# Performance work log

Measured on AMD Instinct MI355X. Metric: run time of the kernel, lower is better.

Reference implementation:

```python
import jax, jax.numpy as jnp
import numpy as np

B, N, E, IN = 16, 4096, 65536, 128
FILTERS = [256, 256, 128]


def setup_inputs() -> dict:
    key = jax.random.key(0)
    ks = jax.random.split(key, 12)
    inp = {
        "x": jax.random.normal(ks[0], (B, N, IN), dtype=jnp.float32),
        "edge_index": jax.random.randint(ks[1], (B, 2, E), 0, N, dtype=jnp.int32),
        "edge_weight": jax.random.uniform(ks[2], (B, E), dtype=jnp.float32),
        "mask": jax.random.randint(ks[3], (B, N), 0, 2, dtype=jnp.int32),
    }
    dims = [IN] + FILTERS
    for i in range(3):
        inp[f"W{i+1}"] = jax.random.normal(ks[4 + 2 * i], (dims[i], dims[i + 1]), dtype=jnp.float32) / np.sqrt(dims[i]).astype(np.float32)
        inp[f"b{i+1}"] = 0.01 * jax.random.normal(ks[5 + 2 * i], (dims[i + 1],), dtype=jnp.float32)
    return inp


def _gcn_layer(x, ei, ew, valid, W, b):
    # GCNConv(add_self_loops=False, normalize=False):
    #   h = x @ W; out[v] = sum_{(u,v)} ew * h[u]; out += b (valid rows only)
    h = x @ W  # [N, d_out]
    u, v = ei[0], ei[1]
    evalid = valid[u] & valid[v]            # drop edges touching masked-out nodes
    w = jnp.where(evalid, ew, 0.0)
    agg = jnp.zeros_like(h).at[v].add(w[:, None] * h[u])
    return jnp.where(valid[:, None], agg + b, 0.0)


def reference(x, edge_index, edge_weight, mask, W1, b1, W2, b2, W3, b3):
    valid = mask > 0  # [B, N] bool
    out = x
    for W, b in ((W1, b1), (W2, b2), (W3, b3)):
        out = jax.vmap(_gcn_layer, in_axes=(0, 0, 0, 0, None, None))(
            out, edge_index, edge_weight, valid, W, b)
        out = jax.nn.relu(out)  # dropout p=0.0 -> identity
    return out
```

## Files before the change

kernel.cpp:

```cpp
#include <hip/hip_runtime.h>

static constexpr int BATCH = 16;
static constexpr int NNODE = 4096;
static constexpr int NEDGE = 65536;
static constexpr int ROWS  = BATCH * NNODE;
static constexpr int CAP   = 2432;
static constexpr int PM    = BATCH * CAP;
static constexpr int DCAP  = 64;

typedef _Float16 half8  __attribute__((ext_vector_type(8)));
typedef _Float16 half4v __attribute__((ext_vector_type(4)));
typedef _Float16 half2v __attribute__((ext_vector_type(2)));
typedef float    f32x4  __attribute__((ext_vector_type(4)));
typedef float    f32x2  __attribute__((ext_vector_type(2)));

__global__ __launch_bounds__(256) void build_kernel(
    const int* __restrict__ ei, const float* __restrict__ ew,
    const int* __restrict__ mask,
    const float* __restrict__ W1, const float* __restrict__ W2,
    const float* __restrict__ W3,
    int* __restrict__ cursor, unsigned int* __restrict__ bkt,
    _Float16* __restrict__ Wt1, _Float16* __restrict__ Wt2,
    _Float16* __restrict__ Wt3,
    int* __restrict__ vlist, int* __restrict__ validN)
{
    __shared__ int sums[256];
    const int blk = blockIdx.x;
    const int t   = threadIdx.x;

    if (blk < 4096) {
        const int idx = blk * 256 + t;
        const int b = idx >> 16;
        const int e = idx & (NEDGE - 1);
        const int* eib = ei + (size_t)b * 2 * NEDGE;
        const int u = eib[e];
        const int v = eib[NEDGE + e];
        const int mrow = b * NNODE;
        if (mask[mrow + u] != 0 && mask[mrow + v] != 0) {
            const _Float16 w = (_Float16)ew[(size_t)b * NEDGE + e];
            const unsigned short wb = __builtin_bit_cast(unsigned short, w);
            const int pos = atomicAdd(&cursor[mrow + v], 1);
            if (pos < DCAP)
                bkt[(size_t)(mrow + v) * DCAP + pos] = ((unsigned)wb << 16) | (unsigned)u;
        }
    } else if (blk < 4608) {
        const int i = (blk - 4096) * 256 + t;
        if (i < 32768) {
            int k = i >> 8, n = i & 255;
            Wt1[n * 128 + k] = (_Float16)W1[i];
        } else if (i < 98304) {
            int j = i - 32768;
            int k = j >> 8, n = j & 255;
            Wt2[n * 256 + k] = (_Float16)W2[j];
        } else {
            int j = i - 98304;
            int k = j >> 7, n = j & 127;
            Wt3[n * 256 + k] = (_Float16)W3[j];
        }
    } else {
        const int b = blk - 4608;
        const int* mb = mask + b * NNODE;
        for (int i = t; i < CAP; i += 256) vlist[b * CAP + i] = 0;

        int loc[16]; int s = 0;
        #pragma unroll
        for (int i = 0; i < 16; ++i) { loc[i] = (mb[t * 16 + i] != 0); s += loc[i]; }
        sums[t] = s;
        __syncthreads();
        for (int off = 1; off < 256; off <<= 1) {
            int v = (t >= off) ? sums[t - off] : 0;
            __syncthreads();
            sums[t] += v;
            __syncthreads();
        }
        int run = (t == 0) ? 0 : sums[t - 1];
        #pragma unroll
        for (int i = 0; i < 16; ++i) {
            const int n = t * 16 + i;
            if (loc[i]) {
                if (run < CAP) vlist[b * CAP + run] = n;
                ++run;
            }
        }
        if (t == 255) validN[b] = run;
    }
}

__global__ __launch_bounds__(256, 4) void fused_g1(
    const unsigned int* __restrict__ bkt, const int* __restrict__ cursor,
    const float* __restrict__ X,
    const int* __restrict__ vlist, const int* __restrict__ validN,
    const _Float16* __restrict__ Wt,
    const float* __restrict__ bias,
    _Float16* __restrict__ Ac)
{
    constexpr int K = 128;
    constexpr int NPAN = 4;
    constexpr int PSTR = 1032;
    constexpr int NW = 64, NI = 4, RST = 72;
    constexpr int NCH = CAP / 32;
    constexpr int ASZ = (NPAN * PSTR) > (4 * 16 * RST) ? (NPAN * PSTR) : (4 * 16 * RST);
    __shared__ _Float16 A16[ASZ];
    __shared__ int s_v[32], s_deg[32];
    __shared__ unsigned s_bk[32][16];

    const int tid  = threadIdx.x;
    const int lane = tid & 63;
    const int wave = tid >> 6;
    const int quad = lane >> 4;
    const int l15  = lane & 15;

    const int xcd  = blockIdx.x & 7;
    const int j    = blockIdx.x >> 3;
    const int batch = 2 * xcd + (j >= NCH);
    const int tile  = (j >= NCH) ? j - NCH : j;
    const int vN   = validN[batch];
    if (tile * 32 >= vN) return;
    const int mrow = batch * NNODE;

    if (tid < 32) {
        const int slot = tile * 32 + tid;
        int v = 0, dg = 0;
        if (slot < vN) {
            v = vlist[batch * CAP + slot];
            dg = cursor[mrow + v];
            dg = dg > DCAP ? DCAP : dg;
        }
        s_v[tid] = v; s_deg[tid] = dg;
    }
    __syncthreads();
    if (tid < 128) {
        const int r = tid >> 2, part = tid & 3;
        const uint4 q = *(const uint4*)&bkt[(size_t)(mrow + s_v[r]) * DCAP + part * 4];
        *(uint4*)&s_bk[r][part * 4] = q;
    }
    __syncthreads();

    const float* Xb = X + (size_t)mrow * 128 + lane * 2;
    for (int r8 = 0; r8 < 8; ++r8) {
        const int r = wave * 8 + r8;
        const int dg = s_deg[r];
        float a0 = 0.0f, a1 = 0.0f;
        if (dg > 0) {
            unsigned pk[16];
            #pragma unroll
            for (int t = 0; t < 16; ++t) pk[t] = s_bk[r][t];
            const unsigned u0 = pk[0] & 0xffffu;
            float wj[16]; float2 xv[16];
            #pragma unroll
            for (int t = 0; t < 16; ++t) {
                const bool ok = (t < dg);
                const unsigned u = ok ? (pk[t] & 0xffffu) : u0;
                wj[t] = ok ? (float)__builtin_bit_cast(_Float16, (unsigned short)(pk[t] >> 16)) : 0.0f;
                xv[t] = *(const float2*)(Xb + (size_t)u * 128);
            }
            #pragma unroll
            for (int t = 0; t < 16; ++t) { a0 += wj[t] * xv[t].x; a1 += wj[t] * xv[t].y; }
            if (dg > 16) {
                const unsigned* bk = bkt + (size_t)(mrow + s_v[r]) * DCAP;
                for (int i = 16; i < dg; ++i) {
                    const unsigned p = bk[i];
                    const float w = (float)__builtin_bit_cast(_Float16, (unsigned short)(p >> 16));
                    const float2 x2 = *(const float2*)(Xb + (size_t)(p & 0xffffu) * 128);
                    a0 += w * x2.x; a1 += w * x2.y;
                }
            }
        }
        half2v o = {(_Float16)a0, (_Float16)a1};
        *(half2v*)&A16[(lane >> 4) * PSTR + r * 32 + ((lane * 2) & 31)] = o;
    }
    __syncthreads();

    f32x4 acc[2][NI];
    #pragma unroll
    for (int mi = 0; mi < 2; ++mi)
        #pragma unroll
        for (int ni = 0; ni < NI; ++ni) acc[mi][ni] = (f32x4)0.0f;

    const _Float16* ap = A16 + l15 * 32 + quad * 8;
    const _Float16* wp = Wt + (size_t)(wave * NW + l15) * K + quad * 8;

    #pragma unroll
    for (int pp = 0; pp < NPAN; ++pp) {
        half8 af[2], bf[NI];
        #pragma unroll
        for (int mi = 0; mi < 2; ++mi)
            af[mi] = *(const half8*)(ap + pp * PSTR + mi * 16 * 32);
        #pragma unroll
        for (int ni = 0; ni < NI; ++ni)
            bf[ni] = *(const half8*)(wp + (size_t)ni * 16 * K + pp * 32);
        #pragma unroll
        for (int mi = 0; mi < 2; ++mi)
            #pragma unroll
            for (int ni = 0; ni < NI; ++ni)
                acc[mi][ni] = __builtin_amdgcn_mfma_f32_16x16x32_f16(
                    bf[ni], af[mi], acc[mi][ni], 0, 0, 0);
    }
    __syncthreads();

    _Float16* stg = A16 + wave * 16 * RST;
    const int rr = lane >> 2;
    const int c0 = lane & 3;
    #pragma unroll
    for (int mi = 0; mi < 2; ++mi) {
        #pragma unroll
        for (int ni = 0; ni < NI; ++ni) {
            f32x4 v = acc[mi][ni];
            const f32x4 bv = *(const f32x4*)&bias[wave * NW + ni * 16 + quad * 4];
            half4v o;
            #pragma unroll
            for (int r = 0; r < 4; ++r) o[r] = (_Float16)fmaxf(v[r] + bv[r], 0.0f);
            *(half4v*)&stg[l15 * RST + ni * 16 + quad * 4] = o;
        }
        const int slot = tile * 32 + mi * 16 + rr;
        if (slot < vN) {
            const int vs = s_v[mi * 16 + rr];
            _Float16* hp2 = &Ac[((size_t)mrow + vs) * 256 + wave * NW];
            #pragma unroll
            for (int c = 0; c < NI / 2; ++c) {
                const int ch = (c0 + 4 * c) * 8;
                half8 v = *(const half8*)&stg[rr * RST + ch];
                *(half8*)(hp2 + ch) = v;
            }
        }
    }
}

__global__ __launch_bounds__(256, 4) void fused_g23(
    const unsigned int* __restrict__ bkt, const int* __restrict__ cursor,
    const _Float16* __restrict__ Ac,
    const int* __restrict__ vlist, const int* __restrict__ validN,
    const _Float16* __restrict__ Wt2,
    const _Float16* __restrict__ Wt3,
    const float* __restrict__ b2,
    _Float16* __restrict__ H3)
{
    constexpr int K    = 256;
    constexpr int NPAN = 8;
    constexpr int PSTR = 1032;
    constexpr int NCH  = CAP / 32;
    __shared__ _Float16 A16[NPAN * PSTR];
    __shared__ int s_v[32], s_deg[32];
    __shared__ unsigned s_bk[32][16];

    const int tid  = threadIdx.x;
    const int lane = tid & 63;
    const int wave = tid >> 6;
    const int quad = lane >> 4;
    const int l15  = lane & 15;

    const int xcd  = blockIdx.x & 7;
    const int j    = blockIdx.x >> 3;
    const int batch = 2 * xcd + (j >= NCH);
    const int tile  = (j >= NCH) ? j - NCH : j;
    const int vN   = validN[batch];
    if (tile * 32 >= vN) return;
    const int mrow = batch * NNODE;

    if (tid < 32) {
        const int slot = tile * 32 + tid;
        int v = 0, dg = 0;
        if (slot < vN) {
            v = vlist[batch * CAP + slot];
            dg = cursor[mrow + v];
            dg = dg > DCAP ? DCAP : dg;
        }
        s_v[tid] = v; s_deg[tid] = dg;
    }
    __syncthreads();
    if (tid < 128) {
        const int r = tid >> 2, part = tid & 3;
        const uint4 q = *(const uint4*)&bkt[(size_t)(mrow + s_v[r]) * DCAP + part * 4];
        *(uint4*)&s_bk[r][part * 4] = q;
    }
    __syncthreads();

    const _Float16* Ab = Ac + (size_t)mrow * 256 + lane * 4;
    for (int r8 = 0; r8 < 8; ++r8) {
        const int r = wave * 8 + r8;
        const int dg = s_deg[r];
        float a0 = 0.0f, a1 = 0.0f, a2 = 0.0f, a3 = 0.0f;
        if (dg > 0) {
            unsigned pk[16];
            #pragma unroll
            for (int t = 0; t < 16; ++t) pk[t] = s_bk[r][t];
            const unsigned u0 = pk[0] & 0xffffu;
            float wj[16]; half4v hv[16];
            #pragma unroll
            for (int t = 0; t < 16; ++t) {
                const bool ok = (t < dg);
                const unsigned u = ok ? (pk[t] & 0xffffu) : u0;
                wj[t] = ok ? (float)__builtin_bit_cast(_Float16, (unsigned short)(pk[t] >> 16)) : 0.0f;
                hv[t] = *(const half4v*)(Ab + (size_t)u * 256);
            }
            #pragma unroll
            for (int t = 0; t < 16; ++t) {
                a0 += wj[t] * (float)hv[t][0];
                a1 += wj[t] * (float)hv[t][1];
                a2 += wj[t] * (float)hv[t][2];
                a3 += wj[t] * (float)hv[t][3];
            }
            if (dg > 16) {
                const unsigned* bk = bkt + (size_t)(mrow + s_v[r]) * DCAP;
                for (int i = 16; i < dg; ++i) {
                    const unsigned p = bk[i];
                    const float w = (float)__builtin_bit_cast(_Float16, (unsigned short)(p >> 16));
                    const half4v h = *(const half4v*)(Ab + (size_t)(p & 0xffffu) * 256);
                    a0 += w * (float)h[0]; a1 += w * (float)h[1];
                    a2 += w * (float)h[2]; a3 += w * (float)h[3];
                }
            }
        }
        half4v o = {(_Float16)a0, (_Float16)a1, (_Float16)a2, (_Float16)a3};
        *(half4v*)&A16[(lane >> 3) * PSTR + r * 32 + ((lane * 4) & 31)] = o;
    }
    __syncthreads();

    f32x4 acc[2][4];
    #pragma unroll
    for (int mi = 0; mi < 2; ++mi)
        #pragma unroll
        for (int ni = 0; ni < 4; ++ni) acc[mi][ni] = (f32x4)0.0f;

    const _Float16* ap = A16 + l15 * 32 + quad * 8;
    const _Float16* wp = Wt2 + (size_t)(wave * 64 + l15) * K + quad * 8;

    #pragma unroll
    for (int pp = 0; pp < NPAN; ++pp) {
        half8 af[2], bf[4];
        #pragma unroll
        for (int mi = 0; mi < 2; ++mi)
            af[mi] = *(const half8*)(ap + pp * PSTR + mi * 16 * 32);
        #pragma unroll
        for (int ni = 0; ni < 4; ++ni)
            bf[ni] = *(const half8*)(wp + (size_t)ni * 16 * K + pp * 32);
        #pragma unroll
        for (int mi = 0; mi < 2; ++mi)
            #pragma unroll
            for (int ni = 0; ni < 4; ++ni)
                acc[mi][ni] = __builtin_amdgcn_mfma_f32_16x16x32_f16(
                    bf[ni], af[mi], acc[mi][ni], 0, 0, 0);
    }
    __syncthreads();

    #pragma unroll
    for (int mi = 0; mi < 2; ++mi) {
        const int row = mi * 16 + l15;
        #pragma unroll
        for (int ni = 0; ni < 4; ++ni) {
            const int col = wave * 64 + ni * 16 + quad * 4;
            const f32x4 bv = *(const f32x4*)&b2[col];
            f32x4 v = acc[mi][ni];
            half4v o;
            #pragma unroll
            for (int r = 0; r < 4; ++r) o[r] = (_Float16)fmaxf(v[r] + bv[r], 0.0f);
            *(half4v*)&A16[(col >> 5) * PSTR + row * 32 + (col & 31)] = o;
        }
    }
    __syncthreads();

    f32x4 acc2[2][2];
    #pragma unroll
    for (int mi = 0; mi < 2; ++mi)
        #pragma unroll
        for (int ni = 0; ni < 2; ++ni) acc2[mi][ni] = (f32x4)0.0f;

    const _Float16* wp3 = Wt3 + (size_t)(wave * 32 + l15) * K + quad * 8;
    #pragma unroll
    for (int pp = 0; pp < NPAN; ++pp) {
        half8 af[2], bf[2];
        #pragma unroll
        for (int mi = 0; mi < 2; ++mi)
            af[mi] = *(const half8*)(ap + pp * PSTR + mi * 16 * 32);
        #pragma unroll
        for (int ni = 0; ni < 2; ++ni)
            bf[ni] = *(const half8*)(wp3 + (size_t)ni * 16 * K + pp * 32);
        #pragma unroll
        for (int mi = 0; mi < 2; ++mi)
            #pragma unroll
            for (int ni = 0; ni < 2; ++ni)
                acc2[mi][ni] = __builtin_amdgcn_mfma_f32_16x16x32_f16(
                    bf[ni], af[mi], acc2[mi][ni], 0, 0, 0);
    }
    __syncthreads();

    constexpr int RST = 40;
    _Float16* stg = A16 + wave * 16 * RST;
    const int rr = lane >> 2;
    const int c0 = lane & 3;
    #pragma unroll
    for (int mi = 0; mi < 2; ++mi) {
        #pragma unroll
        for (int ni = 0; ni < 2; ++ni) {
            f32x4 v = acc2[mi][ni];
            half4v o;
            #pragma unroll
            for (int r = 0; r < 4; ++r) o[r] = (_Float16)v[r];
            *(half4v*)&stg[l15 * RST + ni * 16 + quad * 4] = o;
        }
        const int slot = tile * 32 + mi * 16 + rr;
        if (slot < vN) {
            const int vs = s_v[mi * 16 + rr];
            _Float16* hp2 = &H3[((size_t)mrow + vs) * 128 + wave * 32];
            const int ch = c0 * 8;
            half8 v = *(const half8*)&stg[rr * RST + ch];
            *(half8*)(hp2 + ch) = v;
        }
    }
}

__global__ __launch_bounds__(256) void gather_final(
    const int* __restrict__ cursor, const unsigned int* __restrict__ bkt,
    const _Float16* __restrict__ H3,
    const int* __restrict__ mask, const float* __restrict__ bias,
    float* __restrict__ OUT)
{
    constexpr int NU = NNODE / 4;
    const int tid  = threadIdx.x;
    const int lane = tid & 63;
    const int wave = tid >> 6;

    const int xcd  = blockIdx.x & 7;
    const int jj   = blockIdx.x >> 3;
    const int batch = 2 * xcd + (jj >= NU);
    const int unit  = (jj >= NU) ? jj - NU : jj;

    const int n = unit * 4 + wave;
    const int mrow = batch * NNODE + n;

    float acc[2] = {};
    if (mask[mrow] != 0) {
        int deg = cursor[mrow];
        deg = deg > DCAP ? DCAP : deg;
        const unsigned* bk = bkt + (size_t)mrow * DCAP;
        const _Float16* Hb = H3 + (size_t)batch * NNODE * 128 + lane * 2;

        for (int i = 0; i < deg; i += 8) {
            const int cnt = deg - i;
            unsigned pk[8];
            #pragma unroll
            for (int t = 0; t < 8; ++t) pk[t] = bk[i + t];
            const unsigned u0 = pk[0] & 0xffffu;
            float wj[8]; const _Float16* hp[8];
            #pragma unroll
            for (int t = 0; t < 8; ++t) {
                const bool ok = (t < cnt);
                const unsigned u = ok ? (pk[t] & 0xffffu) : u0;
                wj[t] = ok ? (float)__builtin_bit_cast(_Float16, (unsigned short)(pk[t] >> 16)) : 0.0f;
                hp[t] = Hb + (size_t)u * 128;
            }
            half2v hv[8];
            #pragma unroll
            for (int t = 0; t < 8; ++t) hv[t] = *(const half2v*)hp[t];
            #pragma unroll
            for (int t = 0; t < 8; ++t)
                #pragma unroll
                for (int c = 0; c < 2; ++c) acc[c] += wj[t] * (float)hv[t][c];
        }
        #pragma unroll
        for (int c = 0; c < 2; ++c)
            acc[c] = fmaxf(acc[c] + bias[lane * 2 + c], 0.0f);
    }
    f32x2 o = {acc[0], acc[1]};
    *(f32x2*)&OUT[(size_t)mrow * 128 + lane * 2] = o;
}

extern "C" void kernel_launch(void* const* d_in, const int* in_sizes, int n_in,
                              void* d_out, int out_size, void* d_ws, size_t ws_size,
                              hipStream_t stream) {
    const float* x    = (const float*)d_in[0];
    const int*   ei   = (const int*)  d_in[1];
    const float* ew   = (const float*)d_in[2];
    const int*   mask = (const int*)  d_in[3];
    const float* W1   = (const float*)d_in[4];
    const float* b1   = (const float*)d_in[5];
    const float* W2   = (const float*)d_in[6];
    const float* b2   = (const float*)d_in[7];
    const float* W3   = (const float*)d_in[8];
    const float* b3   = (const float*)d_in[9];
    float* out = (float*)d_out;

    char* ws = (char*)d_ws;
    _Float16* Ac  = (_Float16*)(ws);
    _Float16* H3  = (_Float16*)(ws + (32u << 20));
    unsigned int* bkt = (unsigned int*)(ws + (48u << 20));
    _Float16* Wt1 = (_Float16*)(ws + (64u << 20));
    _Float16* Wt2 = Wt1 + 128 * 256;
    _Float16* Wt3 = Wt2 + 256 * 256;
    int* cursor   = (int*)(Wt3 + 256 * 128);
    int* vlist    = cursor + ROWS;
    int* validN   = vlist + PM;

    const dim3 blk(256);

    hipMemsetAsync(cursor, 0, (size_t)ROWS * sizeof(int), stream);

    build_kernel<<<4624, blk, 0, stream>>>(ei, ew, mask, W1, W2, W3,
                                           cursor, bkt, Wt1, Wt2, Wt3,
                                           vlist, validN);

    const int gemmBlocks = PM / 32;
    const int finBlocks  = ROWS / 4;

    fused_g1<<<gemmBlocks, blk, 0, stream>>>(bkt, cursor, x, vlist, validN,
                                             Wt1, b1, Ac);

    fused_g23<<<gemmBlocks, blk, 0, stream>>>(bkt, cursor, Ac, vlist, validN,
                                              Wt2, Wt3, b2, H3);

    gather_final<<<finBlocks, blk, 0, stream>>>(cursor, bkt, H3, mask, b3, out);
}
```

Baseline: 220.7 us.

## Interleave neighbor gathers across eight rows per wave in fused GCN kernels

```diff
diff --git a/kernel.cpp b/kernel.cpp
--- a/kernel.cpp
+++ b/kernel.cpp
@@ -86,7 +86,7 @@
     }
 }
 
-__global__ __launch_bounds__(256, 4) void fused_g1(
+__global__ __launch_bounds__(256, 3) void fused_g1(
     const unsigned int* __restrict__ bkt, const int* __restrict__ cursor,
     const float* __restrict__ X,
     const int* __restrict__ vlist, const int* __restrict__ validN,
@@ -120,13 +120,13 @@
 
     if (tid < 32) {
         const int slot = tile * 32 + tid;
-        int v = 0, dg = 0;
+        int v = 0, dgv = 0;
         if (slot < vN) {
             v = vlist[batch * CAP + slot];
-            dg = cursor[mrow + v];
-            dg = dg > DCAP ? DCAP : dg;
-        }
-        s_v[tid] = v; s_deg[tid] = dg;
+            dgv = cursor[mrow + v];
+            dgv = dgv > DCAP ? DCAP : dgv;
+        }
+        s_v[tid] = v; s_deg[tid] = dgv;
     }
     __syncthreads();
     if (tid < 128) {
@@ -136,38 +136,57 @@
     }
     __syncthreads();
 
+    const int rbase = wave * 8;
+    int dg[8];
+    #pragma unroll
+    for (int r = 0; r < 8; ++r) dg[r] = s_deg[rbase + r];
+    int mdg = 0;
+    #pragma unroll
+    for (int r = 0; r < 8; ++r) mdg = dg[r] > mdg ? dg[r] : mdg;
+    const int nmain = mdg < 16 ? mdg : 16;
+
     const float* Xb = X + (size_t)mrow * 128 + lane * 2;
-    for (int r8 = 0; r8 < 8; ++r8) {
-        const int r = wave * 8 + r8;
-        const int dg = s_deg[r];
-        float a0 = 0.0f, a1 = 0.0f;
-        if (dg > 0) {
-            unsigned pk[16];
-            #pragma unroll
-            for (int t = 0; t < 16; ++t) pk[t] = s_bk[r][t];
-            const unsigned u0 = pk[0] & 0xffffu;
-            float wj[16]; float2 xv[16];
-            #pragma unroll
-            for (int t = 0; t < 16; ++t) {
-                const bool ok = (t < dg);
-                const unsigned u = ok ? (pk[t] & 0xffffu) : u0;
-                wj[t] = ok ? (float)__builtin_bit_cast(_Float16, (unsigned short)(pk[t] >> 16)) : 0.0f;
-                xv[t] = *(const float2*)(Xb + (size_t)u * 128);
-            }
-            #pragma unroll
-            for (int t = 0; t < 16; ++t) { a0 += wj[t] * xv[t].x; a1 += wj[t] * xv[t].y; }
-            if (dg > 16) {
-                const unsigned* bk = bkt + (size_t)(mrow + s_v[r]) * DCAP;
-                for (int i = 16; i < dg; ++i) {
-                    const unsigned p = bk[i];
-                    const float w = (float)__builtin_bit_cast(_Float16, (unsigned short)(p >> 16));
-                    const float2 x2 = *(const float2*)(Xb + (size_t)(p & 0xffffu) * 128);
-                    a0 += w * x2.x; a1 += w * x2.y;
-                }
-            }
-        }
-        half2v o = {(_Float16)a0, (_Float16)a1};
-        *(half2v*)&A16[(lane >> 4) * PSTR + r * 32 + ((lane * 2) & 31)] = o;
+    f32x2 acc8[8];
+    #pragma unroll
+    for (int r = 0; r < 8; ++r) acc8[r] = (f32x2)0.0f;
+
+    for (int t0 = 0; t0 < nmain; t0 += 2) {
+        float wj[8][2]; float2 xv[8][2];
+        #pragma unroll
+        for (int r = 0; r < 8; ++r)
+            #pragma unroll
+            for (int k = 0; k < 2; ++k) {
+                const unsigned p = s_bk[rbase + r][t0 + k];
+                const unsigned u = p & 0xFFFu;
+                const bool ok = (t0 + k) < dg[r];
+                wj[r][k] = ok ? (float)__builtin_bit_cast(_Float16, (unsigned short)(p >> 16)) : 0.0f;
+                xv[r][k] = *(const float2*)(Xb + (size_t)u * 128);
+            }
+        #pragma unroll
+        for (int r = 0; r < 8; ++r)
+            #pragma unroll
+            for (int k = 0; k < 2; ++k) {
+                acc8[r][0] += wj[r][k] * xv[r][k].x;
+                acc8[r][1] += wj[r][k] * xv[r][k].y;
+            }
+    }
+    if (mdg > 16) {
+        #pragma unroll 1
+        for (int r = 0; r < 8; ++r) {
+            const unsigned* bk2 = bkt + (size_t)(mrow + s_v[rbase + r]) * DCAP;
+            #pragma unroll 1
+            for (int i = 16; i < dg[r]; ++i) {
+                const unsigned p = bk2[i];
+                const float w = (float)__builtin_bit_cast(_Float16, (unsigned short)(p >> 16));
+                const float2 x2 = *(const float2*)(Xb + (size_t)(p & 0xFFFu) * 128);
+                acc8[r][0] += w * x2.x; acc8[r][1] += w * x2.y;
+            }
+        }
+    }
+    #pragma unroll
+    for (int r = 0; r < 8; ++r) {
+        half2v o = {(_Float16)acc8[r][0], (_Float16)acc8[r][1]};
+        *(half2v*)&A16[(lane >> 4) * PSTR + (rbase + r) * 32 + ((lane * 2) & 31)] = o;
     }
     __syncthreads();
 
@@ -226,7 +245,7 @@
     }
 }
 
-__global__ __launch_bounds__(256, 4) void fused_g23(
+__global__ __launch_bounds__(256, 3) void fused_g23(
     const unsigned int* __restrict__ bkt, const int* __restrict__ cursor,
     const _Float16* __restrict__ Ac,
     const int* __restrict__ vlist, const int* __restrict__ validN,
@@ -259,13 +278,13 @@
 
     if (tid < 32) {
         const int slot = tile * 32 + tid;
-        int v = 0, dg = 0;
+        int v = 0, dgv = 0;
         if (slot < vN) {
             v = vlist[batch * CAP + slot];
-            dg = cursor[mrow + v];
-            dg = dg > DCAP ? DCAP : dg;
-        }
-        s_v[tid] = v; s_deg[tid] = dg;
+            dgv = cursor[mrow + v];
+            dgv = dgv > DCAP ? DCAP : dgv;
+        }
+        s_v[tid] = v; s_deg[tid] = dgv;
     }
     __syncthreads();
     if (tid < 128) {
@@ -275,44 +294,62 @@
     }
     __syncthreads();
 
+    const int rbase = wave * 8;
+    const unsigned vsafe = (unsigned)s_v[0];
+    int dg[8];
+    #pragma unroll
+    for (int r = 0; r < 8; ++r) dg[r] = s_deg[rbase + r];
+    int mdg = 0;
+    #pragma unroll
+    for (int r = 0; r < 8; ++r) mdg = dg[r] > mdg ? dg[r] : mdg;
+    const int nmain = mdg < 16 ? mdg : 16;
+
     const _Float16* Ab = Ac + (size_t)mrow * 256 + lane * 4;
-    for (int r8 = 0; r8 < 8; ++r8) {
-        const int r = wave * 8 + r8;
-        const int dg = s_deg[r];
-        float a0 = 0.0f, a1 = 0.0f, a2 = 0.0f, a3 = 0.0f;
-        if (dg > 0) {
-            unsigned pk[16];
-            #pragma unroll
-            for (int t = 0; t < 16; ++t) pk[t] = s_bk[r][t];
-            const unsigned u0 = pk[0] & 0xffffu;
-            float wj[16]; half4v hv[16];
-            #pragma unroll
-            for (int t = 0; t < 16; ++t) {
-                const bool ok = (t < dg);
-                const unsigned u = ok ? (pk[t] & 0xffffu) : u0;
-                wj[t] = ok ? (float)__builtin_bit_cast(_Float16, (unsigned short)(pk[t] >> 16)) : 0.0f;
-                hv[t] = *(const half4v*)(Ab + (size_t)u * 256);
-            }
-            #pragma unroll
-            for (int t = 0; t < 16; ++t) {
-                a0 += wj[t] * (float)hv[t][0];
-                a1 += wj[t] * (float)hv[t][1];
-                a2 += wj[t] * (float)hv[t][2];
-                a3 += wj[t] * (float)hv[t][3];
-            }
-            if (dg > 16) {
-                const unsigned* bk = bkt + (size_t)(mrow + s_v[r]) * DCAP;
-                for (int i = 16; i < dg; ++i) {
-                    const unsigned p = bk[i];
-                    const float w = (float)__builtin_bit_cast(_Float16, (unsigned short)(p >> 16));
-                    const half4v h = *(const half4v*)(Ab + (size_t)(p & 0xffffu) * 256);
-                    a0 += w * (float)h[0]; a1 += w * (float)h[1];
-                    a2 += w * (float)h[2]; a3 += w * (float)h[3];
-                }
-            }
-        }
-        half4v o = {(_Float16)a0, (_Float16)a1, (_Float16)a2, (_Float16)a3};
-        *(half4v*)&A16[(lane >> 3) * PSTR + r * 32 + ((lane * 4) & 31)] = o;
+    f32x4 acc8[8];
+    #pragma unroll
+    for (int r = 0; r < 8; ++r) acc8[r] = (f32x4)0.0f;
+
+    for (int t0 = 0; t0 < nmain; t0 += 2) {
+        float wj[8][2]; half4v hv[8][2];
+        #pragma unroll
+        for (int r = 0; r < 8; ++r)
+            #pragma unroll
+            for (int k = 0; k < 2; ++k) {
+                const unsigned p = s_bk[rbase + r][t0 + k];
+                const bool ok = (t0 + k) < dg[r];
+                const unsigned u = ok ? (p & 0xFFFu) : vsafe;
+                wj[r][k] = ok ? (float)__builtin_bit_cast(_Float16, (unsigned short)(p >> 16)) : 0.0f;
+                hv[r][k] = *(const half4v*)(Ab + (size_t)u * 256);
+            }
+        #pragma unroll
+        for (int r = 0; r < 8; ++r)
+            #pragma unroll
+            for (int k = 0; k < 2; ++k) {
+                acc8[r][0] += wj[r][k] * (float)hv[r][k][0];
+                acc8[r][1] += wj[r][k] * (float)hv[r][k][1];
+                acc8[r][2] += wj[r][k] * (float)hv[r][k][2];
+                acc8[r][3] += wj[r][k] * (float)hv[r][k][3];
+            }
+    }
+    if (mdg > 16) {
+        #pragma unroll 1
+        for (int r = 0; r < 8; ++r) {
+            const unsigned* bk2 = bkt + (size_t)(mrow + s_v[rbase + r]) * DCAP;
+            #pragma unroll 1
+            for (int i = 16; i < dg[r]; ++i) {
+                const unsigned p = bk2[i];
+                const float w = (float)__builtin_bit_cast(_Float16, (unsigned short)(p >> 16));
+                const half4v h = *(const half4v*)(Ab + (size_t)(p & 0xFFFu) * 256);
+                acc8[r][0] += w * (float)h[0]; acc8[r][1] += w * (float)h[1];
+                acc8[r][2] += w * (float)h[2]; acc8[r][3] += w * (float)h[3];
+            }
+        }
+    }
+    #pragma unroll
+    for (int r = 0; r < 8; ++r) {
+        half4v o = {(_Float16)acc8[r][0], (_Float16)acc8[r][1],
+                    (_Float16)acc8[r][2], (_Float16)acc8[r][3]};
+        *(half4v*)&A16[(lane >> 3) * PSTR + (rbase + r) * 32 + ((lane * 4) & 31)] = o;
     }
     __syncthreads();
 
@@ -440,12 +477,12 @@
             unsigned pk[8];
             #pragma unroll
             for (int t = 0; t < 8; ++t) pk[t] = bk[i + t];
-            const unsigned u0 = pk[0] & 0xffffu;
+            const unsigned u0 = pk[0] & 0xFFFu;
             float wj[8]; const _Float16* hp[8];
             #pragma unroll
             for (int t = 0; t < 8; ++t) {
                 const bool ok = (t < cnt);
-                const unsigned u = ok ? (pk[t] & 0xffffu) : u0;
+                const unsigned u = ok ? (pk[t] & 0xFFFu) : u0;
                 wj[t] = ok ? (float)__builtin_bit_cast(_Float16, (unsigned short)(pk[t] >> 16)) : 0.0f;
                 hp[t] = Hb + (size_t)u * 128;
             }
```

Result: no change. 217.9 us (-1.3%).
